# Kernel optimization log

Measured on AMD Instinct MI355X. Metric: run time of the kernel, lower is better.

## Reference

```python
import jax, jax.numpy as jnp
import numpy as np
from jax import lax

B, S, E, SD = 8, 4096, 1024, 8


def setup_inputs() -> dict:
    key = jax.random.key(0)
    ks = jax.random.split(key, 4)
    x = jax.random.normal(ks[0], (B, S, E), dtype=jnp.float32)
    W_in = jax.random.normal(ks[1], (E, E + SD), dtype=jnp.float32) / np.sqrt(E)
    b_in = jnp.zeros((E + SD,), dtype=jnp.float32)
    W_g = jax.random.normal(ks[2], (E + SD, SD), dtype=jnp.float32) / np.sqrt(E + SD)
    b_g = jnp.zeros((SD,), dtype=jnp.float32)
    W_out = jax.random.normal(ks[3], (E + SD, E), dtype=jnp.float32) / np.sqrt(E + SD)
    b_out = jnp.zeros((E,), dtype=jnp.float32)
    return {"x": x, "W_in": W_in, "b_in": b_in, "W_g": W_g, "b_g": b_g,
            "W_out": W_out, "b_out": b_out}


def reference(x, W_in, b_in, W_g, b_g, W_out, b_out):
    embed_dim = W_in.shape[0]
    # State-independent projections batched over the whole sequence.
    combined = jnp.einsum('bse,ec->bsc', x, W_in) + b_in            # [B,S,E+SD]
    embed = combined[..., :embed_dim]                                # [B,S,E]
    state_in = combined[..., embed_dim:]                             # [B,S,SD]
    gate = jax.nn.sigmoid(jnp.einsum('bsc,cd->bsd', combined, W_g) + b_g)  # [B,S,SD]

    # Only the tiny gated state recurrence is sequential.
    def step(state, gs):
        g, si = gs
        new = g * state + (1.0 - g) * si
        return new, new

    state0 = jnp.zeros((x.shape[0], state_in.shape[-1]), dtype=x.dtype)
    g_t = jnp.moveaxis(gate, 1, 0)        # [S,B,SD]
    si_t = jnp.moveaxis(state_in, 1, 0)   # [S,B,SD]
    final_state, states = lax.scan(step, state0, (g_t, si_t))
    states = jnp.moveaxis(states, 0, 1)   # [B,S,SD]

    out = jnp.einsum('bsc,cd->bsd', jnp.concatenate([embed, states], axis=-1), W_out) + b_out
    return out, final_state
```

## Files before the change

kernel.cpp:

```cpp
#include <hip/hip_runtime.h>

typedef unsigned short ushort_t;
typedef __attribute__((ext_vector_type(8))) short short8;
typedef __attribute__((ext_vector_type(4))) float floatx4;

#define B_ 8
#define S_ 4096
#define E_ 1024
#define SD_ 8
#define M_TOTAL (B_ * S_)
#define NC 1032
#define NG 1040
#define NPAD 1152

__device__ __forceinline__ ushort_t f2bf(float f) {
    union { float f; unsigned u; } v; v.f = f;
    unsigned u = v.u;
    unsigned r = (u + 0x7fffu + ((u >> 16) & 1u)) >> 16;
    return (ushort_t)r;
}
__device__ __forceinline__ float bf2f(ushort_t h) {
    union { unsigned u; float f; } v; v.u = ((unsigned)h) << 16;
    return v.f;
}

__device__ __forceinline__ void stage16(ushort_t* lds_base_uniform, const ushort_t* g) {
    __builtin_amdgcn_global_load_lds(
        (const __attribute__((address_space(1))) void*)g,
        (__attribute__((address_space(3))) void*)lds_base_uniform, 16, 0, 0);
}

__global__ void cvt_x4(const float* __restrict__ x, ushort_t* __restrict__ xb) {
    size_t i = ((size_t)blockIdx.x * 256 + threadIdx.x) * 4;
    float4 v = *(const float4*)(x + i);
    ushort4 o;
    o.x = f2bf(v.x); o.y = f2bf(v.y); o.z = f2bf(v.z); o.w = f2bf(v.w);
    *(ushort4*)(xb + i) = o;
}

__global__ void wcomb_kernel(const float* __restrict__ W_in, const float* __restrict__ Wg,
                             float* __restrict__ Wc) {
    const int k = blockIdx.x;
    const int lane = threadIdx.x;
    float acc[8] = {0.f,0.f,0.f,0.f,0.f,0.f,0.f,0.f};
    for (int c = lane; c < NC; c += 64) {
        float w = W_in[(size_t)k * NC + c];
#pragma unroll
        for (int d = 0; d < 8; d++) acc[d] += w * Wg[(size_t)c * 8 + d];
    }
#pragma unroll
    for (int d = 0; d < 8; d++) {
#pragma unroll
        for (int off = 32; off >= 1; off >>= 1) acc[d] += __shfl_xor(acc[d], off);
    }
    if (lane == 0) {
#pragma unroll
        for (int d = 0; d < 8; d++) Wc[k * 8 + d] = acc[d];
    }
}

__global__ void bias_ext_kernel(const float* __restrict__ b_in, const float* __restrict__ Wg,
                                const float* __restrict__ bg, float* __restrict__ be) {
    int c = blockIdx.x * 256 + threadIdx.x;
    if (c >= NPAD) return;
    if (c < NC) { be[c] = b_in[c]; return; }
    if (c < NG) {
        int d = c - NC;
        float s = bg[d];
        for (int j = 0; j < NC; j++) s += b_in[j] * Wg[(size_t)j * 8 + d];
        be[c] = s;
        return;
    }
    be[c] = 0.f;
}

__global__ void prep_win(const float* __restrict__ W, const float* __restrict__ Wc,
                         ushort_t* __restrict__ WT) {
    int idx = blockIdx.x * 256 + threadIdx.x;
    int n = idx >> 10, k = idx & 1023;
    float v;
    if (n < NC)       v = W[(size_t)k * NC + n];
    else if (n < NG)  v = Wc[k * 8 + (n - NC)];
    else              v = 0.f;
    WT[idx] = f2bf(v);
}

__global__ void prep_wout(const float* __restrict__ W, ushort_t* __restrict__ WT) {
    int idx = blockIdx.x * 256 + threadIdx.x;
    int n = idx / NPAD, k = idx - n * NPAD;
    WT[idx] = (k < NC) ? f2bf(W[(size_t)k * E_ + n]) : (ushort_t)0;
}

template <bool OUT_BF16>
__global__ __launch_bounds__(256, 2) void gemm_bt(
    const ushort_t* __restrict__ A, const ushort_t* __restrict__ BT,
    void* __restrict__ Cout, const float* __restrict__ bias,
    int K, int lda, int ldb, int ldc)
{
    __shared__ __align__(16) ushort_t sA[128 * 32];
    __shared__ __align__(16) ushort_t sB[128 * 32];
    const int tid = threadIdx.x;
    const int wave = tid >> 6;
    const int lane = tid & 63;

    const int gx = gridDim.x;
    int flat = blockIdx.y * gx + blockIdx.x;
    const int band_size = 8 * gx;
    int band = flat / band_size;
    int r = flat - band * band_size;
    const int m0 = (band * 8 + (r & 7)) * 128;
    const int n0 = (r >> 3) * 128;

    const int wm = wave >> 1, wn = wave & 1;
    const int fr = lane & 15, fq = lane >> 4;
    const int sr = lane >> 2;
    const int sc = (lane & 3) * 8;

    floatx4 acc[4][4];
#pragma unroll
    for (int i = 0; i < 4; i++)
#pragma unroll
        for (int j = 0; j < 4; j++) acc[i][j] = (floatx4)0.f;

    const ushort_t* gA = A + (size_t)(m0 + wave * 32 + sr) * lda + sc;
    const ushort_t* gB = BT + (size_t)(n0 + wave * 32 + sr) * ldb + sc;

    for (int k0 = 0; k0 < K; k0 += 32) {
        __syncthreads();
        stage16(&sA[(wave * 32 + 0) * 32], gA + k0);
        stage16(&sA[(wave * 32 + 16) * 32], gA + (size_t)16 * lda + k0);
        stage16(&sB[(wave * 32 + 0) * 32], gB + k0);
        stage16(&sB[(wave * 32 + 16) * 32], gB + (size_t)16 * ldb + k0);
        __syncthreads();

        short8 a[4], b[4];
#pragma unroll
        for (int i = 0; i < 4; i++)
            a[i] = *(const short8*)&sA[(wm * 64 + i * 16 + fr) * 32 + fq * 8];
#pragma unroll
        for (int j = 0; j < 4; j++)
            b[j] = *(const short8*)&sB[(wn * 64 + j * 16 + fr) * 32 + fq * 8];
#pragma unroll
        for (int i = 0; i < 4; i++)
#pragma unroll
            for (int j = 0; j < 4; j++)
                acc[i][j] = __builtin_amdgcn_mfma_f32_16x16x32_bf16(a[i], b[j], acc[i][j], 0, 0, 0);
    }

#pragma unroll
    for (int i = 0; i < 4; i++) {
        int row = m0 + wm * 64 + i * 16 + fq * 4;
#pragma unroll
        for (int j = 0; j < 4; j++) {
            int col = n0 + wn * 64 + j * 16 + fr;
            float bv = bias[col];
#pragma unroll
            for (int r2 = 0; r2 < 4; r2++) {
                float v = acc[i][j][r2] + bv;
                if (OUT_BF16)
                    ((ushort_t*)Cout)[(size_t)(row + r2) * ldc + col] = f2bf(v);
                else
                    ((float*)Cout)[(size_t)(row + r2) * ldc + col] = v;
            }
        }
    }
}

__global__ void scan_chunks(const ushort_t* __restrict__ combined,
                            float* __restrict__ chA, float* __restrict__ chB)
{
    const int c = blockIdx.x, lane = threadIdx.x;
    const int b = lane >> 3, d = lane & 7;
    float A = 1.f, Bv = 0.f;
    const int s0 = c * 64;
    for (int s = s0; s < s0 + 64; s++) {
        size_t m = (size_t)b * S_ + s;
        float z = bf2f(combined[m * NPAD + NC + d]);
        float g = 1.f / (1.f + __expf(-z));
        float si = bf2f(combined[m * NPAD + E_ + d]);
        Bv = g * Bv + (1.f - g) * si;
        A *= g;
    }
    chA[c * 64 + lane] = A;
    chB[c * 64 + lane] = Bv;
}

__global__ void scan_apply(ushort_t* __restrict__ combined,
                           const float* __restrict__ chA, const float* __restrict__ chB,
                           float* __restrict__ final_state)
{
    const int c = blockIdx.x, lane = threadIdx.x;
    const int b = lane >> 3, d = lane & 7;
    float state = 0.f;
    for (int j = 0; j < c; j++)
        state = chA[j * 64 + lane] * state + chB[j * 64 + lane];
    const int s0 = c * 64;
    for (int s = s0; s < s0 + 64; s++) {
        size_t m = (size_t)b * S_ + s;
        float z = bf2f(combined[m * NPAD + NC + d]);
        float g = 1.f / (1.f + __expf(-z));
        float si = bf2f(combined[m * NPAD + E_ + d]);
        state = g * state + (1.f - g) * si;
        combined[m * NPAD + E_ + d] = f2bf(state);
    }
    if (c == 63) final_state[lane] = state;
}

extern "C" void kernel_launch(void* const* d_in, const int* in_sizes, int n_in,
                              void* d_out, int out_size, void* d_ws, size_t ws_size,
                              hipStream_t stream)
{
    (void)in_sizes; (void)n_in; (void)out_size; (void)ws_size;
    const float* x     = (const float*)d_in[0];
    const float* W_in  = (const float*)d_in[1];
    const float* b_in  = (const float*)d_in[2];
    const float* W_g   = (const float*)d_in[3];
    const float* b_g   = (const float*)d_in[4];
    const float* W_out = (const float*)d_in[5];
    const float* b_out = (const float*)d_in[6];

    ushort_t* combined = (ushort_t*)d_ws;
    ushort_t* WinT  = combined + (size_t)M_TOTAL * NPAD;
    ushort_t* WoutT = WinT + (size_t)NPAD * E_;
    float* Wc   = (float*)(WoutT + (size_t)E_ * NPAD);
    float* be   = Wc + 1024 * 8;
    float* chA  = be + NPAD;
    float* chB  = chA + 64 * 64;

    ushort_t* xb = (ushort_t*)d_out;
    float* outp = (float*)d_out;
    float* fs = outp + (size_t)M_TOTAL * E_;

    cvt_x4<<<(M_TOTAL * E_) / 1024, 256, 0, stream>>>(x, xb);
    wcomb_kernel<<<E_, 64, 0, stream>>>(W_in, W_g, Wc);
    bias_ext_kernel<<<(NPAD + 255) / 256, 256, 0, stream>>>(b_in, W_g, b_g, be);
    prep_win<<<(NPAD * E_) / 256, 256, 0, stream>>>(W_in, Wc, WinT);
    prep_wout<<<(E_ * NPAD) / 256, 256, 0, stream>>>(W_out, WoutT);

    gemm_bt<true><<<dim3(NPAD / 128, M_TOTAL / 128), 256, 0, stream>>>(
        xb, WinT, combined, be, E_, E_, E_, NPAD);

    scan_chunks<<<64, 64, 0, stream>>>(combined, chA, chB);
    scan_apply<<<64, 64, 0, stream>>>(combined, chA, chB, fs);

    gemm_bt<false><<<dim3(E_ / 128, M_TOTAL / 128), 256, 0, stream>>>(
        combined, WoutT, outp, b_out, NPAD, NPAD, NPAD, E_);
}
```

Measured before the change: 502.6 us.

## Fold W_in embed block into W_out to remove the intermediate combined GEMM

Precomputes W_in[:, :E] @ W_out[:E] as a single E×E weight, so the output is x @ Wbig plus a small K=32 correction from the scan states. This replaces the large first GEMM (M×1152×1024) and its bf16 round trip of the combined tensor with a skinny 16-column MFMA kernel for state_in and the gate logits. The scan now runs with more chunks over a compact 32-wide buffer. The trade-offs are an extra 1024³ weight GEMM per call and different rounding, since embed is no longer rounded to bf16 before the output projection.

```diff
diff --git a/kernel.cpp b/kernel.cpp
--- a/kernel.cpp
+++ b/kernel.cpp
@@ -10,8 +10,8 @@
 #define SD_ 8
 #define M_TOTAL (B_ * S_)
 #define NC 1032
-#define NG 1040
-#define NPAD 1152
+#define NCH 256
+#define CHS (S_ / NCH)
 
 __device__ __forceinline__ ushort_t f2bf(float f) {
     union { float f; unsigned u; } v; v.f = f;
@@ -59,43 +59,66 @@
     }
 }
 
-__global__ void bias_ext_kernel(const float* __restrict__ b_in, const float* __restrict__ Wg,
-                                const float* __restrict__ bg, float* __restrict__ be) {
-    int c = blockIdx.x * 256 + threadIdx.x;
-    if (c >= NPAD) return;
-    if (c < NC) { be[c] = b_in[c]; return; }
-    if (c < NG) {
-        int d = c - NC;
-        float s = bg[d];
-        for (int j = 0; j < NC; j++) s += b_in[j] * Wg[(size_t)j * 8 + d];
-        be[c] = s;
-        return;
-    }
-    be[c] = 0.f;
-}
-
-__global__ void prep_win(const float* __restrict__ W, const float* __restrict__ Wc,
-                         ushort_t* __restrict__ WT) {
+__global__ void prep_winb(const float* __restrict__ W, ushort_t* __restrict__ O) {
+    int i = blockIdx.x * 256 + threadIdx.x;
+    int k = i >> 8, j0 = (i & 255) * 4;
+    float4 v = *(const float4*)(W + (size_t)k * NC + j0);
+    ushort4 o;
+    o.x = f2bf(v.x); o.y = f2bf(v.y); o.z = f2bf(v.z); o.w = f2bf(v.w);
+    *(ushort4*)(O + (size_t)k * E_ + j0) = o;
+}
+
+__global__ void prep_wouts(const float* __restrict__ W, ushort_t* __restrict__ O) {
     int idx = blockIdx.x * 256 + threadIdx.x;
-    int n = idx >> 10, k = idx & 1023;
-    float v;
-    if (n < NC)       v = W[(size_t)k * NC + n];
-    else if (n < NG)  v = Wc[k * 8 + (n - NC)];
-    else              v = 0.f;
-    WT[idx] = f2bf(v);
-}
-
-__global__ void prep_wout(const float* __restrict__ W, ushort_t* __restrict__ WT) {
+    int n = idx >> 10, j = idx & 1023;
+    O[idx] = f2bf(W[(size_t)j * E_ + n]);
+}
+
+__global__ void prep_small(const float* __restrict__ W_in, const float* __restrict__ Wc,
+                           const float* __restrict__ W_out, const float* __restrict__ b_in,
+                           const float* __restrict__ Wg, const float* __restrict__ bg,
+                           ushort_t* __restrict__ BT16, ushort_t* __restrict__ WoutT2,
+                           float* __restrict__ bias16) {
     int idx = blockIdx.x * 256 + threadIdx.x;
-    int n = idx / NPAD, k = idx - n * NPAD;
-    WT[idx] = (k < NC) ? f2bf(W[(size_t)k * E_ + n]) : (ushort_t)0;
-}
-
-template <bool OUT_BF16>
+    if (idx < 32768) {
+        int n = idx >> 10, k = idx & 1023;
+        float v;
+        if (n < 8)        v = W_in[(size_t)k * NC + 1024 + n];
+        else if (n < 16)  v = Wc[k * 8 + (n - 8)];
+        else              v = 0.f;
+        BT16[idx] = f2bf(v);
+    } else {
+        int i2 = idx - 32768;
+        int n = i2 >> 5, k2 = i2 & 31;
+        float v = (k2 < 8) ? W_out[(size_t)(1024 + k2) * E_ + n] : 0.f;
+        WoutT2[i2] = f2bf(v);
+    }
+    if (idx < 32) {
+        float s;
+        if (idx < 8) s = b_in[1024 + idx];
+        else if (idx < 16) {
+            int d = idx - 8;
+            s = bg[d];
+            for (int j = 0; j < NC; j++) s += b_in[j] * Wg[(size_t)j * 8 + d];
+        } else s = 0.f;
+        bias16[idx] = s;
+    }
+}
+
+__global__ void bias2_kernel(const float* __restrict__ b_in, const float* __restrict__ W_out,
+                             const float* __restrict__ b_out, float* __restrict__ bias2) {
+    int n = blockIdx.x * 64 + threadIdx.x;
+    float acc = b_out[n];
+    for (int j = 0; j < E_; j++) acc += b_in[j] * W_out[(size_t)j * E_ + n];
+    bias2[n] = acc;
+}
+
+template <bool OUT_BF16, bool EXTRA>
 __global__ __launch_bounds__(256, 2) void gemm_bt(
     const ushort_t* __restrict__ A, const ushort_t* __restrict__ BT,
+    const ushort_t* __restrict__ A2, const ushort_t* __restrict__ BT2,
     void* __restrict__ Cout, const float* __restrict__ bias,
-    int K, int lda, int ldb, int ldc)
+    int K, int lda, int ldb, int lda2, int ldb2, int ldc)
 {
     __shared__ __align__(16) ushort_t sA[128 * 32];
     __shared__ __align__(16) ushort_t sB[128 * 32];
@@ -147,13 +170,37 @@
                 acc[i][j] = __builtin_amdgcn_mfma_f32_16x16x32_bf16(a[i], b[j], acc[i][j], 0, 0, 0);
     }
 
+    if constexpr (EXTRA) {
+        const ushort_t* gA2 = A2 + (size_t)(m0 + wave * 32 + sr) * lda2 + sc;
+        const ushort_t* gB2 = BT2 + (size_t)(n0 + wave * 32 + sr) * ldb2 + sc;
+        __syncthreads();
+        stage16(&sA[(wave * 32 + 0) * 32], gA2);
+        stage16(&sA[(wave * 32 + 16) * 32], gA2 + (size_t)16 * lda2);
+        stage16(&sB[(wave * 32 + 0) * 32], gB2);
+        stage16(&sB[(wave * 32 + 16) * 32], gB2 + (size_t)16 * ldb2);
+        __syncthreads();
+
+        short8 a[4], b[4];
+#pragma unroll
+        for (int i = 0; i < 4; i++)
+            a[i] = *(const short8*)&sA[(wm * 64 + i * 16 + fr) * 32 + fq * 8];
+#pragma unroll
+        for (int j = 0; j < 4; j++)
+            b[j] = *(const short8*)&sB[(wn * 64 + j * 16 + fr) * 32 + fq * 8];
+#pragma unroll
+        for (int i = 0; i < 4; i++)
+#pragma unroll
+            for (int j = 0; j < 4; j++)
+                acc[i][j] = __builtin_amdgcn_mfma_f32_16x16x32_bf16(a[i], b[j], acc[i][j], 0, 0, 0);
+    }
+
 #pragma unroll
     for (int i = 0; i < 4; i++) {
         int row = m0 + wm * 64 + i * 16 + fq * 4;
 #pragma unroll
         for (int j = 0; j < 4; j++) {
             int col = n0 + wn * 64 + j * 16 + fr;
-            float bv = bias[col];
+            float bv = bias ? bias[col] : 0.f;
 #pragma unroll
             for (int r2 = 0; r2 < 4; r2++) {
                 float v = acc[i][j][r2] + bv;
@@ -166,18 +213,43 @@
     }
 }
 
-__global__ void scan_chunks(const ushort_t* __restrict__ combined,
+__global__ __launch_bounds__(256) void skinny16(
+    const ushort_t* __restrict__ A,
+    const ushort_t* __restrict__ BT,
+    const float* __restrict__ bias,
+    ushort_t* __restrict__ C)
+{
+    const int tid = threadIdx.x, wave = tid >> 6, lane = tid & 63;
+    const int m0 = blockIdx.x * 64 + wave * 16;
+    const int fr = lane & 15, fq = lane >> 4;
+    floatx4 acc0 = (floatx4)0.f;
+    const ushort_t* pa  = A + (size_t)(m0 + fr) * E_ + fq * 8;
+    const ushort_t* pb0 = BT + (size_t)fr * E_ + fq * 8;
+    for (int k0 = 0; k0 < E_; k0 += 32) {
+        short8 a  = *(const short8*)(pa + k0);
+        short8 b0 = *(const short8*)(pb0 + k0);
+        acc0 = __builtin_amdgcn_mfma_f32_16x16x32_bf16(a, b0, acc0, 0, 0, 0);
+    }
+#pragma unroll
+    for (int r = 0; r < 4; r++) {
+        int row = m0 + fq * 4 + r;
+        C[(size_t)row * 32 + fr]      = f2bf(acc0[r] + bias[fr]);
+        C[(size_t)row * 32 + 16 + fr] = (ushort_t)0;
+    }
+}
+
+__global__ void scan_chunks(const ushort_t* __restrict__ comb,
                             float* __restrict__ chA, float* __restrict__ chB)
 {
     const int c = blockIdx.x, lane = threadIdx.x;
     const int b = lane >> 3, d = lane & 7;
     float A = 1.f, Bv = 0.f;
-    const int s0 = c * 64;
-    for (int s = s0; s < s0 + 64; s++) {
+    const int s0 = c * CHS;
+    for (int s = s0; s < s0 + CHS; s++) {
         size_t m = (size_t)b * S_ + s;
-        float z = bf2f(combined[m * NPAD + NC + d]);
+        float z = bf2f(comb[m * 32 + 8 + d]);
         float g = 1.f / (1.f + __expf(-z));
-        float si = bf2f(combined[m * NPAD + E_ + d]);
+        float si = bf2f(comb[m * 32 + d]);
         Bv = g * Bv + (1.f - g) * si;
         A *= g;
     }
@@ -185,7 +257,7 @@
     chB[c * 64 + lane] = Bv;
 }
 
-__global__ void scan_apply(ushort_t* __restrict__ combined,
+__global__ void scan_apply(ushort_t* __restrict__ comb,
                            const float* __restrict__ chA, const float* __restrict__ chB,
                            float* __restrict__ final_state)
 {
@@ -194,16 +266,16 @@
     float state = 0.f;
     for (int j = 0; j < c; j++)
         state = chA[j * 64 + lane] * state + chB[j * 64 + lane];
-    const int s0 = c * 64;
-    for (int s = s0; s < s0 + 64; s++) {
+    const int s0 = c * CHS;
+    for (int s = s0; s < s0 + CHS; s++) {
         size_t m = (size_t)b * S_ + s;
-        float z = bf2f(combined[m * NPAD + NC + d]);
+        float z = bf2f(comb[m * 32 + 8 + d]);
         float g = 1.f / (1.f + __expf(-z));
-        float si = bf2f(combined[m * NPAD + E_ + d]);
+        float si = bf2f(comb[m * 32 + d]);
         state = g * state + (1.f - g) * si;
-        combined[m * NPAD + E_ + d] = f2bf(state);
-    }
-    if (c == 63) final_state[lane] = state;
+        comb[m * 32 + d] = f2bf(state);
+    }
+    if (c == NCH - 1) final_state[lane] = state;
 }
 
 extern "C" void kernel_launch(void* const* d_in, const int* in_sizes, int n_in,
@@ -219,30 +291,37 @@
     const float* W_out = (const float*)d_in[5];
     const float* b_out = (const float*)d_in[6];
 
-    ushort_t* combined = (ushort_t*)d_ws;
-    ushort_t* WinT  = combined + (size_t)M_TOTAL * NPAD;
-    ushort_t* WoutT = WinT + (size_t)NPAD * E_;
-    float* Wc   = (float*)(WoutT + (size_t)E_ * NPAD);
-    float* be   = Wc + 1024 * 8;
-    float* chA  = be + NPAD;
-    float* chB  = chA + 64 * 64;
-
-    ushort_t* xb = (ushort_t*)d_out;
+    ushort_t* xb     = (ushort_t*)d_ws;
+    ushort_t* comb16 = xb + (size_t)M_TOTAL * E_;
+    ushort_t* WbigT  = comb16 + (size_t)M_TOTAL * 32;
+    ushort_t* Winb   = WbigT + (size_t)E_ * E_;
+    ushort_t* WoutTa = Winb + (size_t)E_ * E_;
+    ushort_t* WoutT2 = WoutTa + (size_t)E_ * E_;
+    ushort_t* BT16   = WoutT2 + (size_t)E_ * 32;
+    float*    Wc     = (float*)(BT16 + (size_t)32 * E_);
+    float*    bias16 = Wc + 1024 * 8;
+    float*    bias2v = bias16 + 32;
+    float*    chA    = bias2v + E_;
+    float*    chB    = chA + NCH * 64;
+
     float* outp = (float*)d_out;
     float* fs = outp + (size_t)M_TOTAL * E_;
 
     cvt_x4<<<(M_TOTAL * E_) / 1024, 256, 0, stream>>>(x, xb);
     wcomb_kernel<<<E_, 64, 0, stream>>>(W_in, W_g, Wc);
-    bias_ext_kernel<<<(NPAD + 255) / 256, 256, 0, stream>>>(b_in, W_g, b_g, be);
-    prep_win<<<(NPAD * E_) / 256, 256, 0, stream>>>(W_in, Wc, WinT);
-    prep_wout<<<(E_ * NPAD) / 256, 256, 0, stream>>>(W_out, WoutT);
-
-    gemm_bt<true><<<dim3(NPAD / 128, M_TOTAL / 128), 256, 0, stream>>>(
-        xb, WinT, combined, be, E_, E_, E_, NPAD);
-
-    scan_chunks<<<64, 64, 0, stream>>>(combined, chA, chB);
-    scan_apply<<<64, 64, 0, stream>>>(combined, chA, chB, fs);
-
-    gemm_bt<false><<<dim3(E_ / 128, M_TOTAL / 128), 256, 0, stream>>>(
-        combined, WoutT, outp, b_out, NPAD, NPAD, NPAD, E_);
-}
+    prep_winb<<<1024, 256, 0, stream>>>(W_in, Winb);
+    prep_wouts<<<(E_ * E_) / 256, 256, 0, stream>>>(W_out, WoutTa);
+    prep_small<<<256, 256, 0, stream>>>(W_in, Wc, W_out, b_in, W_g, b_g, BT16, WoutT2, bias16);
+    bias2_kernel<<<E_ / 64, 64, 0, stream>>>(b_in, W_out, b_out, bias2v);
+
+    gemm_bt<true, false><<<dim3(E_ / 128, E_ / 128), 256, 0, stream>>>(
+        WoutTa, Winb, nullptr, nullptr, WbigT, nullptr, E_, E_, E_, 0, 0, E_);
+
+    skinny16<<<M_TOTAL / 64, 256, 0, stream>>>(xb, BT16, bias16, comb16);
+
+    scan_chunks<<<NCH, 64, 0, stream>>>(comb16, chA, chB);
+    scan_apply<<<NCH, 64, 0, stream>>>(comb16, chA, chB, fs);
+
+    gemm_bt<false, true><<<dim3(E_ / 128, M_TOTAL / 128), 256, 0, stream>>>(
+        xb, WbigT, comb16, WoutT2, outp, bias2v, E_, E_, E_, 32, 32, E_);
+}
```

Result: faster. 490.2 us (-2.5%).
